# Kernel tuning notes

Hardware: AMD Instinct MI355X
Metric: run time of the kernel (lower is better)

Reference implementation:

```python
import jax, jax.numpy as jnp
import numpy as np

B, TE, T = 128, 256, 200
H, PRE, MEL, R = 256, 128, 80, 5
OUT = MEL * R  # 400


def _gru(x, h, wih, whh, bih, bhh):
    # PyTorch GRUCell math. wih: [3H, in], whh: [3H, H]
    gi = x @ wih.T + bih
    gh = h @ whh.T + bhh
    ir, iz, inn = jnp.split(gi, 3, axis=-1)
    hr, hz, hn = jnp.split(gh, 3, axis=-1)
    r = jax.nn.sigmoid(ir + hr)
    z = jax.nn.sigmoid(iz + hz)
    n = jnp.tanh(inn + r * hn)
    return (1.0 - z) * n + z * h


def setup_inputs() -> dict:
    key = jax.random.key(0)
    ks = jax.random.split(key, 32)
    s = 0.05
    d = {
        "encoder_outputs": jax.random.normal(ks[0], (B, TE, H), jnp.float32),
        "targets": jax.random.normal(ks[1], (B, T, OUT), jnp.float32),
        # prenet (note: prenet input is mel_dim*r = 400 frames fed through Linear(400->256)
        # is not in the original; original hardcodes Linear(256,256) on a 400-dim frame --
        # a bug. We size the first prenet layer to the actual frame dim 400.)
        "prenet_w1": jax.random.normal(ks[2], (H, OUT), jnp.float32) * s,
        "prenet_b1": jnp.zeros((H,), jnp.float32),
        "prenet_w2": jax.random.normal(ks[3], (PRE, H), jnp.float32) * s,
        "prenet_b2": jnp.zeros((PRE,), jnp.float32),
        # attention RNN: GRUCell(256+128, 256)
        "attn_wih": jax.random.normal(ks[4], (3 * H, H + PRE), jnp.float32) * s,
        "attn_whh": jax.random.normal(ks[5], (3 * H, H), jnp.float32) * s,
        "attn_bih": jnp.zeros((3 * H,), jnp.float32),
        "attn_bhh": jnp.zeros((3 * H,), jnp.float32),
        # Bahdanau attention: query layer, memory layer (bias-free), score vector v
        "wq": jax.random.normal(ks[6], (H, H), jnp.float32) * s,
        "wm": jax.random.normal(ks[7], (H, H), jnp.float32) * s,
        "v_attn": jax.random.normal(ks[8], (H,), jnp.float32) * s,
        # proj_to_decoder: Linear(512, 256)
        "wp": jax.random.normal(ks[9], (H, 2 * H), jnp.float32) * s,
        "bp": jnp.zeros((H,), jnp.float32),
        # decoder GRUCell x2 (256,256)
        "g1_wih": jax.random.normal(ks[10], (3 * H, H), jnp.float32) * s,
        "g1_whh": jax.random.normal(ks[11], (3 * H, H), jnp.float32) * s,
        "g1_bih": jnp.zeros((3 * H,), jnp.float32),
        "g1_bhh": jnp.zeros((3 * H,), jnp.float32),
        "g2_wih": jax.random.normal(ks[12], (3 * H, H), jnp.float32) * s,
        "g2_whh": jax.random.normal(ks[13], (3 * H, H), jnp.float32) * s,
        "g2_bih": jnp.zeros((3 * H,), jnp.float32),
        "g2_bhh": jnp.zeros((3 * H,), jnp.float32),
        # proj_to_mel: Linear(256, mel_dim*r)
        "wo": jax.random.normal(ks[14], (OUT, H), jnp.float32) * s,
        "bo": jnp.zeros((OUT,), jnp.float32),
    }
    return d


def reference(encoder_outputs, targets, prenet_w1, prenet_b1, prenet_w2, prenet_b2,
              attn_wih, attn_whh, attn_bih, attn_bhh, wq, wm, v_attn, wp, bp,
              g1_wih, g1_whh, g1_bih, g1_bhh, g2_wih, g2_whh, g2_bih, g2_bhh,
              wo, bo):
    b = encoder_outputs.shape[0]
    # precompute processed memory once (original memory_layer)
    pm = encoder_outputs @ wm.T  # [B, Te, H]

    # teacher-forced previous frames: go-frame (zeros) then targets[:, :-1]
    prev = jnp.concatenate([jnp.zeros((b, 1, OUT), encoder_outputs.dtype),
                            targets[:, :-1]], axis=1)  # [B, T, OUT]
    prev = jnp.swapaxes(prev, 0, 1)  # [T, B, OUT]

    def step(carry, frame):
        attn_h, h1, h2, attn_val = carry
        # prenet (dropout in eval mode -> identity)
        p = jax.nn.relu(frame @ prenet_w1.T + prenet_b1)
        p = jax.nn.relu(p @ prenet_w2.T + prenet_b2)  # [B, 128]
        # attention RNN
        x = jnp.concatenate([p, attn_val], axis=-1)  # [B, 384]
        attn_h = _gru(x, attn_h, attn_wih, attn_whh, attn_bih, attn_bhh)
        # Bahdanau additive attention
        q = attn_h @ wq.T  # [B, H]
        e = jnp.einsum('bth,h->bt', jnp.tanh(pm + q[:, None, :]), v_attn)  # [B, Te]
        align = jax.nn.softmax(e, axis=-1)
        attn_val = jnp.einsum('bt,bth->bh', align, encoder_outputs)
        # decoder RNNs with residual connections
        dec_in = jnp.concatenate([attn_h, attn_val], axis=-1) @ wp.T + bp
        h1 = _gru(dec_in, h1, g1_wih, g1_whh, g1_bih, g1_bhh)
        dec_in = h1 + dec_in
        h2 = _gru(dec_in, h2, g2_wih, g2_whh, g2_bih, g2_bhh)
        dec_in = h2 + dec_in
        out = dec_in @ wo.T + bo  # [B, OUT]
        return (attn_h, h1, h2, attn_val), (out, align)

    z = jnp.zeros((b, H), encoder_outputs.dtype)
    init = (z, z, z, z)
    _, (outs, aligns) = jax.lax.scan(step, init, prev)
    outputs = jnp.swapaxes(outs, 0, 1)      # [B, T, mel_dim*r]
    alignments = jnp.swapaxes(aligns, 0, 1)  # [B, T, Te]
    return outputs, alignments
```

## Files before the change

kernel.cpp:

```cpp
#include <hip/hip_runtime.h>

#define B_    128
#define T_    200
#define TE_   256
#define H_    256
#define PRE_  128
#define OUT_  400
#define BT_   (B_*T_)

__device__ __forceinline__ float sigm_(float x){ return 1.f/(1.f+__expf(-x)); }
__device__ __forceinline__ float tanh_(float x){
  x = fminf(15.f, fmaxf(-15.f, x));
  float e = __expf(2.f*x);
  return 1.f - 2.f/(e+1.f);
}
__device__ __forceinline__ float b2f_lo(unsigned u){ return __uint_as_float(u << 16); }
__device__ __forceinline__ float b2f_hi(unsigned u){ return __uint_as_float(u & 0xffff0000u); }
__device__ __forceinline__ unsigned short f2b(float f){
  unsigned u = __float_as_uint(f);
  unsigned r = (u + 0x7fff + ((u >> 16) & 1)) >> 16;
  return (unsigned short)r;
}

struct TD { const float* src; void* dst; int N; int Ksrc; int col0; int Keff; int bf16; int blk0; };
struct TDs { TD d[13]; };

__global__ __launch_bounds__(256) void transpose_cast(TDs P)
{
  int bid = blockIdx.x, m = 0;
#pragma unroll
  for (int i = 1; i < 13; ++i) if (bid >= P.d[i].blk0) m = i;
  TD t = P.d[m];
  long gid = (long)(bid - t.blk0)*256 + threadIdx.x;
  long nk = (long)t.N * t.Keff;
  if (gid >= nk) return;
  int k = (int)(gid / t.N);
  int j = (int)(gid % t.N);
  float v = t.src[(size_t)j*t.Ksrc + t.col0 + k];
  if (t.bf16) ((unsigned short*)t.dst)[(size_t)k*t.N + j] = f2b(v);
  else        ((float*)t.dst)[(size_t)k*t.N + j] = v;
}

template<int AMODE, bool RELU, int OUTMODE>
__global__ __launch_bounds__(256) void gemm_k(const float* __restrict__ A, int lda,
                                              const float* __restrict__ WT, int N, int K,
                                              const float* __restrict__ bias,
                                              float* __restrict__ C)
{
  const int tid  = threadIdx.x;
  const int row0 = blockIdx.x * 64;
  const int n0   = blockIdx.y * 64;
  __shared__ float As[16][68];
  __shared__ float Bs[16][64];
  const int tx = tid & 15, ty = tid >> 4;
  float acc[4][4];
#pragma unroll
  for (int i = 0; i < 4; ++i)
#pragma unroll
    for (int j = 0; j < 4; ++j) acc[i][j] = 0.f;

  for (int k0 = 0; k0 < K; k0 += 16){
#pragma unroll
    for (int l = 0; l < 4; ++l){
      int idx = tid + l*256;
      int m = idx >> 4, kk = idx & 15;
      float v;
      if (AMODE == 1){
        int r = row0 + m;
        int t = r % T_;
        v = (t == 0) ? 0.f : A[(size_t)(r-1)*OUT_ + k0 + kk];
      } else {
        v = A[(size_t)(row0+m)*lda + k0 + kk];
      }
      As[kk][m] = v;
    }
#pragma unroll
    for (int l = 0; l < 4; ++l){
      int idx = tid + l*256;
      int kk = idx >> 6, j = idx & 63;
      int jg = n0 + j;
      Bs[kk][j] = (jg < N) ? WT[(size_t)(k0+kk)*N + jg] : 0.f;
    }
    __syncthreads();
#pragma unroll
    for (int kk = 0; kk < 16; ++kk){
      float4 a4 = *(const float4*)&As[kk][ty*4];
      float4 b4 = *(const float4*)&Bs[kk][tx*4];
      acc[0][0] = fmaf(a4.x, b4.x, acc[0][0]); acc[0][1] = fmaf(a4.x, b4.y, acc[0][1]);
      acc[0][2] = fmaf(a4.x, b4.z, acc[0][2]); acc[0][3] = fmaf(a4.x, b4.w, acc[0][3]);
      acc[1][0] = fmaf(a4.y, b4.x, acc[1][0]); acc[1][1] = fmaf(a4.y, b4.y, acc[1][1]);
      acc[1][2] = fmaf(a4.y, b4.z, acc[1][2]); acc[1][3] = fmaf(a4.y, b4.w, acc[1][3]);
      acc[2][0] = fmaf(a4.z, b4.x, acc[2][0]); acc[2][1] = fmaf(a4.z, b4.y, acc[2][1]);
      acc[2][2] = fmaf(a4.z, b4.z, acc[2][2]); acc[2][3] = fmaf(a4.z, b4.w, acc[2][3]);
      acc[3][0] = fmaf(a4.w, b4.x, acc[3][0]); acc[3][1] = fmaf(a4.w, b4.y, acc[3][1]);
      acc[3][2] = fmaf(a4.w, b4.z, acc[3][2]); acc[3][3] = fmaf(a4.w, b4.w, acc[3][3]);
    }
    __syncthreads();
  }
#pragma unroll
  for (int i = 0; i < 4; ++i){
    int r = row0 + ty*4 + i;
#pragma unroll
    for (int jj = 0; jj < 4; ++jj){
      int c = n0 + tx*4 + jj;
      if (c < N){
        float v = acc[i][jj] + (bias ? bias[c] : 0.f);
        if (RELU) v = fmaxf(v, 0.f);
        if (OUTMODE == 0){
          C[(size_t)r*N + c] = v;
        } else {
          int b = r / TE_, te = r % TE_;
          C[((size_t)b*H_ + c)*TE_ + te] = v;
        }
      }
    }
  }
}

__device__ __forceinline__ void mv768(const uint2* __restrict__ w,
                                      const float* __restrict__ sin_,
                                      float* __restrict__ part, int tid)
{
  if (tid >= 768) return;
  const int kg = tid / 192;
  const int jt = tid - kg*192;
  const float4* sin4 = (const float4*)sin_;
  const uint2* wp_ = w + (size_t)(kg*64)*192 + jt;
  float a0=0.f, a1=0.f, a2=0.f, a3=0.f;
#pragma unroll 4
  for (int k4 = 0; k4 < 16; ++k4){
    float4 x = sin4[kg*16 + k4];
    uint2 w0 = wp_[0], w1 = wp_[192], w2 = wp_[384], w3 = wp_[576];
    wp_ += 768;
    a0 = fmaf(x.x, b2f_lo(w0.x), a0); a1 = fmaf(x.x, b2f_hi(w0.x), a1);
    a2 = fmaf(x.x, b2f_lo(w0.y), a2); a3 = fmaf(x.x, b2f_hi(w0.y), a3);
    a0 = fmaf(x.y, b2f_lo(w1.x), a0); a1 = fmaf(x.y, b2f_hi(w1.x), a1);
    a2 = fmaf(x.y, b2f_lo(w1.y), a2); a3 = fmaf(x.y, b2f_hi(w1.y), a3);
    a0 = fmaf(x.z, b2f_lo(w2.x), a0); a1 = fmaf(x.z, b2f_hi(w2.x), a1);
    a2 = fmaf(x.z, b2f_lo(w2.y), a2); a3 = fmaf(x.z, b2f_hi(w2.y), a3);
    a0 = fmaf(x.w, b2f_lo(w3.x), a0); a1 = fmaf(x.w, b2f_hi(w3.x), a1);
    a2 = fmaf(x.w, b2f_lo(w3.y), a2); a3 = fmaf(x.w, b2f_hi(w3.y), a3);
  }
  float* pp = part + kg*768 + jt*4;
  pp[0]=a0; pp[1]=a1; pp[2]=a2; pp[3]=a3;
}

template<int KCH>
__device__ __forceinline__ void mv256(const uint2* __restrict__ w,
                                      const float* __restrict__ sin_,
                                      float* __restrict__ part, int tid)
{
  const int kg = tid >> 6;
  const int jt = tid & 63;
  const float4* sin4 = (const float4*)sin_;
  const uint2* wp_ = w + (size_t)(kg*KCH)*64 + jt;
  float a0=0.f, a1=0.f, a2=0.f, a3=0.f;
#pragma unroll
  for (int k4 = 0; k4 < KCH/4; ++k4){
    float4 x = sin4[(kg*KCH)/4 + k4];
    uint2 w0 = wp_[0], w1 = wp_[64], w2 = wp_[128], w3 = wp_[192];
    wp_ += 256;
    a0 = fmaf(x.x, b2f_lo(w0.x), a0); a1 = fmaf(x.x, b2f_hi(w0.x), a1);
    a2 = fmaf(x.x, b2f_lo(w0.y), a2); a3 = fmaf(x.x, b2f_hi(w0.y), a3);
    a0 = fmaf(x.y, b2f_lo(w1.x), a0); a1 = fmaf(x.y, b2f_hi(w1.x), a1);
    a2 = fmaf(x.y, b2f_lo(w1.y), a2); a3 = fmaf(x.y, b2f_hi(w1.y), a3);
    a0 = fmaf(x.z, b2f_lo(w2.x), a0); a1 = fmaf(x.z, b2f_hi(w2.x), a1);
    a2 = fmaf(x.z, b2f_lo(w2.y), a2); a3 = fmaf(x.z, b2f_hi(w2.y), a3);
    a0 = fmaf(x.w, b2f_lo(w3.x), a0); a1 = fmaf(x.w, b2f_hi(w3.x), a1);
    a2 = fmaf(x.w, b2f_lo(w3.y), a2); a3 = fmaf(x.w, b2f_hi(w3.y), a3);
  }
  float* pp = part + kg*256 + jt*4;
  pp[0]=a0; pp[1]=a1; pp[2]=a2; pp[3]=a3;
}

struct DP {
  const float *enc, *preGI, *pm;
  const unsigned short *awihA, *awhh, *wq, *wp, *g1wih, *g1whh, *g2wih, *g2whh;
  const float *abhh, *g1bih, *g1bhh, *g2bih, *g2bhh, *bp, *v_attn;
  float *decbuf, *aln;
};

__global__ __launch_bounds__(1024) void decoder_kernel(DP P)
{
  const int tid = threadIdx.x;
  const int b = blockIdx.x;

  __shared__ __align__(16) float s_ah[H_], s_h1[H_], s_h2[H_], s_av[H_], s_q[H_], s_al[TE_], s_dec[H_];
  __shared__ __align__(16) float s_xc[2*H_];
  __shared__ __align__(16) float s_gi[3*H_], s_gh[3*H_];
  __shared__ __align__(16) float s_pA[4096];
  __shared__ __align__(16) float s_pB[3072];
  __shared__ float s_bhh[3*H_], s_1bi[3*H_], s_1bh[3*H_], s_2bi[3*H_], s_2bh[3*H_];
  __shared__ float s_bp[H_], s_v[H_];
  __shared__ float s_red[8];

  if (tid < H_){
    s_ah[tid]=0.f; s_h1[tid]=0.f; s_h2[tid]=0.f; s_av[tid]=0.f;
    s_bp[tid]=P.bp[tid]; s_v[tid]=P.v_attn[tid];
  }
  if (tid < 3*H_){
    s_bhh[tid]=P.abhh[tid];
    s_1bi[tid]=P.g1bih[tid]; s_1bh[tid]=P.g1bhh[tid];
    s_2bi[tid]=P.g2bih[tid]; s_2bh[tid]=P.g2bhh[tid];
  }
  __syncthreads();

  const float* preg  = P.preGI + (size_t)b*T_*3*H_;
  const float4* pm4  = (const float4*)(P.pm  + (size_t)b*H_*TE_);
  const float4* enc4 = (const float4*)(P.enc + (size_t)b*TE_*H_);
  float* aln_b = P.aln + (size_t)b*T_*TE_;
  float* dec_b = P.decbuf + (size_t)b*T_*H_;

  const uint2* awihA2 = (const uint2*)P.awihA;
  const uint2* awhh2  = (const uint2*)P.awhh;
  const uint2* wq2    = (const uint2*)P.wq;
  const uint2* wp2    = (const uint2*)P.wp;
  const uint2* g1wih2 = (const uint2*)P.g1wih;
  const uint2* g1whh2 = (const uint2*)P.g1whh;
  const uint2* g2wih2 = (const uint2*)P.g2wih;
  const uint2* g2whh2 = (const uint2*)P.g2whh;

  for (int t = 0; t < T_; ++t){
    float gin = (tid < 768) ? preg[(size_t)t*768 + tid] : 0.f;
    mv768(awihA2, s_av, s_pA, tid);
    mv768(awhh2,  s_ah, s_pB, tid);
    __syncthreads();
    if (tid < 768){
      s_gi[tid] = s_pA[tid]+s_pA[768+tid]+s_pA[1536+tid]+s_pA[2304+tid] + gin;
      s_gh[tid] = s_pB[tid]+s_pB[768+tid]+s_pB[1536+tid]+s_pB[2304+tid] + s_bhh[tid];
    }
    __syncthreads();
    if (tid < H_){
      float r = sigm_(s_gi[tid]      + s_gh[tid]);
      float z = sigm_(s_gi[H_+tid]   + s_gh[H_+tid]);
      float n = tanh_(s_gi[2*H_+tid] + r*s_gh[2*H_+tid]);
      s_ah[tid] = (1.f-z)*n + z*s_ah[tid];
    }
    __syncthreads();
    mv256<16>(wq2, s_ah, s_pA, tid);
    __syncthreads();
    if (tid < H_){
      float q = 0.f;
#pragma unroll
      for (int g = 0; g < 16; ++g) q += s_pA[g*256 + tid];
      s_q[tid] = q;
    }
    __syncthreads();
    {
      const int kg = tid >> 6, jt = tid & 63;
      float a0=0.f,a1=0.f,a2=0.f,a3=0.f;
#pragma unroll 4
      for (int hh = 0; hh < 16; ++hh){
        int h = kg*16 + hh;
        float4 pv = pm4[h*64 + jt];
        float qh = s_q[h], vh = s_v[h];
        a0 = fmaf(vh, tanh_(pv.x + qh), a0);
        a1 = fmaf(vh, tanh_(pv.y + qh), a1);
        a2 = fmaf(vh, tanh_(pv.z + qh), a2);
        a3 = fmaf(vh, tanh_(pv.w + qh), a3);
      }
      float* pp = s_pA + kg*256 + jt*4;
      pp[0]=a0; pp[1]=a1; pp[2]=a2; pp[3]=a3;
    }
    __syncthreads();
    float e = 0.f, ex = 0.f;
    if (tid < TE_){
#pragma unroll
      for (int g = 0; g < 16; ++g) e += s_pA[g*256 + tid];
      float m = e;
      for (int o = 32; o; o >>= 1) m = fmaxf(m, __shfl_down(m, o, 64));
      if ((tid & 63) == 0) s_red[tid >> 6] = m;
    }
    __syncthreads();
    if (tid < TE_){
      float m = fmaxf(fmaxf(s_red[0],s_red[1]), fmaxf(s_red[2],s_red[3]));
      ex = __expf(e - m);
      float s = ex;
      for (int o = 32; o; o >>= 1) s += __shfl_down(s, o, 64);
      if ((tid & 63) == 0) s_red[4 + (tid >> 6)] = s;
    }
    __syncthreads();
    if (tid < TE_){
      float s = (s_red[4]+s_red[5])+(s_red[6]+s_red[7]);
      float al = ex / s;
      s_al[tid] = al;
      aln_b[(size_t)t*TE_ + tid] = al;
    }
    __syncthreads();
    {
      const int kg = tid >> 6, jt = tid & 63;
      float a0=0.f,a1=0.f,a2=0.f,a3=0.f;
#pragma unroll 4
      for (int tt = 0; tt < 16; ++tt){
        int te = kg*16 + tt;
        float alv = s_al[te];
        float4 ev = enc4[te*64 + jt];
        a0 = fmaf(alv, ev.x, a0);
        a1 = fmaf(alv, ev.y, a1);
        a2 = fmaf(alv, ev.z, a2);
        a3 = fmaf(alv, ev.w, a3);
      }
      float* pp = s_pA + kg*256 + jt*4;
      pp[0]=a0; pp[1]=a1; pp[2]=a2; pp[3]=a3;
    }
    __syncthreads();
    if (tid < H_){
      float av = 0.f;
#pragma unroll
      for (int g = 0; g < 16; ++g) av += s_pA[g*256 + tid];
      s_av[tid] = av;
      s_xc[tid] = s_ah[tid];
      s_xc[H_ + tid] = av;
    }
    __syncthreads();
    mv256<32>(wp2, s_xc, s_pA, tid);
    __syncthreads();
    if (tid < H_){
      float d = s_bp[tid];
#pragma unroll
      for (int g = 0; g < 16; ++g) d += s_pA[g*256 + tid];
      s_dec[tid] = d;
    }
    __syncthreads();
    mv768(g1wih2, s_dec, s_pA, tid);
    mv768(g1whh2, s_h1,  s_pB, tid);
    __syncthreads();
    if (tid < 768){
      s_gi[tid] = s_pA[tid]+s_pA[768+tid]+s_pA[1536+tid]+s_pA[2304+tid] + s_1bi[tid];
      s_gh[tid] = s_pB[tid]+s_pB[768+tid]+s_pB[1536+tid]+s_pB[2304+tid] + s_1bh[tid];
    }
    __syncthreads();
    if (tid < H_){
      float r = sigm_(s_gi[tid]      + s_gh[tid]);
      float z = sigm_(s_gi[H_+tid]   + s_gh[H_+tid]);
      float n = tanh_(s_gi[2*H_+tid] + r*s_gh[2*H_+tid]);
      float h1n = (1.f-z)*n + z*s_h1[tid];
      s_h1[tid] = h1n;
      s_dec[tid] += h1n;
    }
    __syncthreads();
    mv768(g2wih2, s_dec, s_pA, tid);
    mv768(g2whh2, s_h2,  s_pB, tid);
    __syncthreads();
    if (tid < 768){
      s_gi[tid] = s_pA[tid]+s_pA[768+tid]+s_pA[1536+tid]+s_pA[2304+tid] + s_2bi[tid];
      s_gh[tid] = s_pB[tid]+s_pB[768+tid]+s_pB[1536+tid]+s_pB[2304+tid] + s_2bh[tid];
    }
    __syncthreads();
    if (tid < H_){
      float r = sigm_(s_gi[tid]      + s_gh[tid]);
      float z = sigm_(s_gi[H_+tid]   + s_gh[H_+tid]);
      float n = tanh_(s_gi[2*H_+tid] + r*s_gh[2*H_+tid]);
      float h2n = (1.f-z)*n + z*s_h2[tid];
      s_h2[tid] = h2n;
      float d = s_dec[tid] + h2n;
      s_dec[tid] = d;
      dec_b[(size_t)t*H_ + tid] = d;
    }
    __syncthreads();
  }
}

extern "C" void kernel_launch(void* const* d_in, const int* in_sizes, int n_in,
                              void* d_out, int out_size, void* d_ws, size_t ws_size,
                              hipStream_t stream)
{
  const float* enc   = (const float*)d_in[0];
  const float* tgt   = (const float*)d_in[1];
  const float* pw1   = (const float*)d_in[2];
  const float* pb1   = (const float*)d_in[3];
  const float* pw2   = (const float*)d_in[4];
  const float* pb2   = (const float*)d_in[5];
  const float* awih  = (const float*)d_in[6];
  const float* awhh  = (const float*)d_in[7];
  const float* abih  = (const float*)d_in[8];
  const float* abhh  = (const float*)d_in[9];
  const float* wq    = (const float*)d_in[10];
  const float* wm    = (const float*)d_in[11];
  const float* vat   = (const float*)d_in[12];
  const float* wp    = (const float*)d_in[13];
  const float* bp    = (const float*)d_in[14];
  const float* g1wih = (const float*)d_in[15];
  const float* g1whh = (const float*)d_in[16];
  const float* g1bih = (const float*)d_in[17];
  const float* g1bhh = (const float*)d_in[18];
  const float* g2wih = (const float*)d_in[19];
  const float* g2whh = (const float*)d_in[20];
  const float* g2bih = (const float*)d_in[21];
  const float* g2bhh = (const float*)d_in[22];
  const float* wo    = (const float*)d_in[23];
  const float* bo    = (const float*)d_in[24];

  float* ws = (float*)d_ws;
  size_t off = 0;
  auto alloc = [&](size_t n){ float* p = ws + off; off += (n + 3) & ~(size_t)3; return p; };

  float* wmT    = alloc(65536);
  float* w1T    = alloc(102400);
  float* w2T    = alloc(32768);
  float* awihPT = alloc(98304);
  float* woT    = alloc(102400);
  unsigned short* awihA16 = (unsigned short*)alloc(98304);
  unsigned short* awhh16  = (unsigned short*)alloc(98304);
  unsigned short* wq16    = (unsigned short*)alloc(32768);
  unsigned short* wp16    = (unsigned short*)alloc(65536);
  unsigned short* g1wih16 = (unsigned short*)alloc(98304);
  unsigned short* g1whh16 = (unsigned short*)alloc(98304);
  unsigned short* g2wih16 = (unsigned short*)alloc(98304);
  unsigned short* g2whh16 = (unsigned short*)alloc(98304);
  float* pmf    = alloc((size_t)B_*H_*TE_);
  float* decb   = alloc((size_t)BT_*H_);
  float* preGIf = alloc((size_t)BT_*3*H_);
  float* p1f = decb;
  float* p2f = pmf;

  TDs td;
  const float* srcs[13] = { wm,  pw1, pw2, awih, wo,  awih, awhh, wq,  wp,  g1wih, g1whh, g2wih, g2whh };
  void* dsts[13] = { wmT, w1T, w2T, awihPT, woT, awihA16, awhh16, wq16, wp16, g1wih16, g1whh16, g2wih16, g2whh16 };
  int   Ns[13]   = { 256, 256, 128, 768,  400, 768, 768, 256, 256, 768, 768, 768, 768 };
  int   Kss[13]  = { 256, 400, 256, 384,  256, 384, 256, 256, 512, 256, 256, 256, 256 };
  int   c0s[13]  = { 0,   0,   0,   0,    0,   128, 0,   0,   0,   0,   0,   0,   0 };
  int   Kes[13]  = { 256, 400, 256, 128,  256, 256, 256, 256, 512, 256, 256, 256, 256 };
  int   bfs[13]  = { 0,   0,   0,   0,    0,   1,   1,   1,   1,   1,   1,   1,   1 };
  int blk = 0;
  for (int i = 0; i < 13; ++i){
    td.d[i] = { srcs[i], dsts[i], Ns[i], Kss[i], c0s[i], Kes[i], bfs[i], blk };
    long nk = (long)Ns[i]*Kes[i];
    blk += (int)((nk + 255) / 256);
  }
  transpose_cast<<<blk, 256, 0, stream>>>(td);

  gemm_k<1, true, 0><<<dim3(BT_/64, 4), 256, 0, stream>>>(tgt, 0,   w1T,    256, 400, pb1,  p1f);
  gemm_k<0, true, 0><<<dim3(BT_/64, 2), 256, 0, stream>>>(p1f, 256, w2T,    128, 256, pb2,  p2f);
  gemm_k<0, false,0><<<dim3(BT_/64,12), 256, 0, stream>>>(p2f, 128, awihPT, 768, 128, abih, preGIf);
  gemm_k<0, false,1><<<dim3((B_*TE_)/64, 4), 256, 0, stream>>>(enc, 256, wmT, 256, 256, nullptr, pmf);

  DP P;
  P.enc = enc; P.preGI = preGIf; P.pm = pmf;
  P.awihA = awihA16; P.awhh = awhh16; P.wq = wq16; P.wp = wp16;
  P.g1wih = g1wih16; P.g1whh = g1whh16; P.g2wih = g2wih16; P.g2whh = g2whh16;
  P.abhh = abhh; P.g1bih = g1bih; P.g1bhh = g1bhh; P.g2bih = g2bih; P.g2bhh = g2bhh;
  P.bp = bp; P.v_attn = vat;
  P.decbuf = decb;
  P.aln = (float*)d_out + (size_t)BT_*OUT_;
  decoder_kernel<<<B_, 1024, 0, stream>>>(P);

  gemm_k<0, false,0><<<dim3(BT_/64, 7), 256, 0, stream>>>(decb, 256, woT, 400, 256, bo, (float*)d_out);
}
```

Measured before the change: 13.64 ms.

## Restructure decoder step: batch independent matvecs, bf16 memory/encoder, drop softmax max

The decoder step now issues the attention and both decoder hidden-to-hidden matvecs together in one phase, computes the query and the attention-state half of the projection together, and prefetches the precomputed gate inputs with the otherwise idle threads. This removes several barriers per timestep. The processed memory and the encoder outputs are stored as bf16 to halve per-step global traffic, and biases are kept in registers. The softmax max-subtraction pass is dropped, which saves one reduction and barrier but risks overflow if scores grow large, and bf16 storage lowers precision.

```diff
diff --git a/kernel.cpp b/kernel.cpp
--- a/kernel.cpp
+++ b/kernel.cpp
@@ -22,14 +22,18 @@
   return (unsigned short)r;
 }
 
+#define Q4(xv, wv, A0,A1,A2,A3) \
+  A0=fmaf(xv,b2f_lo(wv.x),A0); A1=fmaf(xv,b2f_hi(wv.x),A1); \
+  A2=fmaf(xv,b2f_lo(wv.y),A2); A3=fmaf(xv,b2f_hi(wv.y),A3);
+
 struct TD { const float* src; void* dst; int N; int Ksrc; int col0; int Keff; int bf16; int blk0; };
-struct TDs { TD d[13]; };
+struct TDs { TD d[14]; };
 
 __global__ __launch_bounds__(256) void transpose_cast(TDs P)
 {
   int bid = blockIdx.x, m = 0;
 #pragma unroll
-  for (int i = 1; i < 13; ++i) if (bid >= P.d[i].blk0) m = i;
+  for (int i = 1; i < 14; ++i) if (bid >= P.d[i].blk0) m = i;
   TD t = P.d[m];
   long gid = (long)(bid - t.blk0)*256 + threadIdx.x;
   long nk = (long)t.N * t.Keff;
@@ -63,16 +67,16 @@
 #pragma unroll
     for (int l = 0; l < 4; ++l){
       int idx = tid + l*256;
-      int m = idx >> 4, kk = idx & 15;
+      int m2 = idx >> 4, kk = idx & 15;
       float v;
       if (AMODE == 1){
-        int r = row0 + m;
+        int r = row0 + m2;
         int t = r % T_;
         v = (t == 0) ? 0.f : A[(size_t)(r-1)*OUT_ + k0 + kk];
       } else {
-        v = A[(size_t)(row0+m)*lda + k0 + kk];
+        v = A[(size_t)(row0+m2)*lda + k0 + kk];
       }
-      As[kk][m] = v;
+      As[kk][m2] = v;
     }
 #pragma unroll
     for (int l = 0; l < 4; ++l){
@@ -108,73 +112,111 @@
         if (RELU) v = fmaxf(v, 0.f);
         if (OUTMODE == 0){
           C[(size_t)r*N + c] = v;
+        } else if (OUTMODE == 1){
+          int b = r / TE_, te = r % TE_;
+          C[((size_t)b*H_ + c)*TE_ + te] = v;
         } else {
           int b = r / TE_, te = r % TE_;
-          C[((size_t)b*H_ + c)*TE_ + te] = v;
+          ((unsigned short*)C)[((size_t)b*H_ + c)*TE_ + te] = f2b(v);
         }
       }
     }
   }
 }
 
-__device__ __forceinline__ void mv768(const uint2* __restrict__ w,
-                                      const float* __restrict__ sin_,
-                                      float* __restrict__ part, int tid)
-{
-  if (tid >= 768) return;
-  const int kg = tid / 192;
-  const int jt = tid - kg*192;
-  const float4* sin4 = (const float4*)sin_;
-  const uint2* wp_ = w + (size_t)(kg*64)*192 + jt;
-  float a0=0.f, a1=0.f, a2=0.f, a3=0.f;
+__device__ __forceinline__ void mv768_pair(const uint2* __restrict__ wA, const uint2* __restrict__ wB,
+                                           const float* __restrict__ xA, const float* __restrict__ xB,
+                                           float* __restrict__ outA, float* __restrict__ outB,
+                                           int kg, int jt)
+{
+  const float4* xa4 = (const float4*)xA;
+  const float4* xb4 = (const float4*)xB;
+  const uint2* pA = wA + (size_t)(kg*64)*192 + jt;
+  const uint2* pB = wB + (size_t)(kg*64)*192 + jt;
+  float a0=0,a1=0,a2=0,a3=0, c0=0,c1=0,c2=0,c3=0;
 #pragma unroll 4
   for (int k4 = 0; k4 < 16; ++k4){
-    float4 x = sin4[kg*16 + k4];
-    uint2 w0 = wp_[0], w1 = wp_[192], w2 = wp_[384], w3 = wp_[576];
-    wp_ += 768;
-    a0 = fmaf(x.x, b2f_lo(w0.x), a0); a1 = fmaf(x.x, b2f_hi(w0.x), a1);
-    a2 = fmaf(x.x, b2f_lo(w0.y), a2); a3 = fmaf(x.x, b2f_hi(w0.y), a3);
-    a0 = fmaf(x.y, b2f_lo(w1.x), a0); a1 = fmaf(x.y, b2f_hi(w1.x), a1);
-    a2 = fmaf(x.y, b2f_lo(w1.y), a2); a3 = fmaf(x.y, b2f_hi(w1.y), a3);
-    a0 = fmaf(x.z, b2f_lo(w2.x), a0); a1 = fmaf(x.z, b2f_hi(w2.x), a1);
-    a2 = fmaf(x.z, b2f_lo(w2.y), a2); a3 = fmaf(x.z, b2f_hi(w2.y), a3);
-    a0 = fmaf(x.w, b2f_lo(w3.x), a0); a1 = fmaf(x.w, b2f_hi(w3.x), a1);
-    a2 = fmaf(x.w, b2f_lo(w3.y), a2); a3 = fmaf(x.w, b2f_hi(w3.y), a3);
-  }
-  float* pp = part + kg*768 + jt*4;
-  pp[0]=a0; pp[1]=a1; pp[2]=a2; pp[3]=a3;
-}
-
-template<int KCH>
-__device__ __forceinline__ void mv256(const uint2* __restrict__ w,
-                                      const float* __restrict__ sin_,
-                                      float* __restrict__ part, int tid)
-{
-  const int kg = tid >> 6;
-  const int jt = tid & 63;
-  const float4* sin4 = (const float4*)sin_;
-  const uint2* wp_ = w + (size_t)(kg*KCH)*64 + jt;
-  float a0=0.f, a1=0.f, a2=0.f, a3=0.f;
-#pragma unroll
-  for (int k4 = 0; k4 < KCH/4; ++k4){
-    float4 x = sin4[(kg*KCH)/4 + k4];
-    uint2 w0 = wp_[0], w1 = wp_[64], w2 = wp_[128], w3 = wp_[192];
-    wp_ += 256;
-    a0 = fmaf(x.x, b2f_lo(w0.x), a0); a1 = fmaf(x.x, b2f_hi(w0.x), a1);
-    a2 = fmaf(x.x, b2f_lo(w0.y), a2); a3 = fmaf(x.x, b2f_hi(w0.y), a3);
-    a0 = fmaf(x.y, b2f_lo(w1.x), a0); a1 = fmaf(x.y, b2f_hi(w1.x), a1);
-    a2 = fmaf(x.y, b2f_lo(w1.y), a2); a3 = fmaf(x.y, b2f_hi(w1.y), a3);
-    a0 = fmaf(x.z, b2f_lo(w2.x), a0); a1 = fmaf(x.z, b2f_hi(w2.x), a1);
-    a2 = fmaf(x.z, b2f_lo(w2.y), a2); a3 = fmaf(x.z, b2f_hi(w2.y), a3);
-    a0 = fmaf(x.w, b2f_lo(w3.x), a0); a1 = fmaf(x.w, b2f_hi(w3.x), a1);
-    a2 = fmaf(x.w, b2f_lo(w3.y), a2); a3 = fmaf(x.w, b2f_hi(w3.y), a3);
-  }
-  float* pp = part + kg*256 + jt*4;
-  pp[0]=a0; pp[1]=a1; pp[2]=a2; pp[3]=a3;
+    float4 x1 = xa4[kg*16+k4];
+    float4 x2 = xb4[kg*16+k4];
+    uint2 wa0=pA[0],wa1=pA[192],wa2=pA[384],wa3=pA[576]; pA += 768;
+    uint2 wb0=pB[0],wb1=pB[192],wb2=pB[384],wb3=pB[576]; pB += 768;
+    Q4(x1.x, wa0, a0,a1,a2,a3) Q4(x1.y, wa1, a0,a1,a2,a3)
+    Q4(x1.z, wa2, a0,a1,a2,a3) Q4(x1.w, wa3, a0,a1,a2,a3)
+    Q4(x2.x, wb0, c0,c1,c2,c3) Q4(x2.y, wb1, c0,c1,c2,c3)
+    Q4(x2.z, wb2, c0,c1,c2,c3) Q4(x2.w, wb3, c0,c1,c2,c3)
+  }
+  *(float4*)(outA + jt*4) = make_float4(a0,a1,a2,a3);
+  *(float4*)(outB + jt*4) = make_float4(c0,c1,c2,c3);
+}
+
+__device__ __forceinline__ void mv768_single(const uint2* __restrict__ w,
+                                             const float* __restrict__ x,
+                                             float* __restrict__ out, int kg, int jt)
+{
+  const float4* x4 = (const float4*)x;
+  const uint2* p = w + (size_t)(kg*64)*192 + jt;
+  float a0=0,a1=0,a2=0,a3=0;
+#pragma unroll 4
+  for (int k4 = 0; k4 < 16; ++k4){
+    float4 x1 = x4[kg*16+k4];
+    uint2 w0=p[0],w1=p[192],w2=p[384],w3=p[576]; p += 768;
+    Q4(x1.x, w0, a0,a1,a2,a3) Q4(x1.y, w1, a0,a1,a2,a3)
+    Q4(x1.z, w2, a0,a1,a2,a3) Q4(x1.w, w3, a0,a1,a2,a3)
+  }
+  *(float4*)(out + jt*4) = make_float4(a0,a1,a2,a3);
+}
+
+__device__ __forceinline__ void mv256_pair(const uint2* __restrict__ wA, const uint2* __restrict__ wB,
+                                           const float* __restrict__ x,
+                                           float* __restrict__ outA, float* __restrict__ outB,
+                                           int kg, int jt)
+{
+  const float4* x4 = (const float4*)x;
+  const uint2* pA = wA + (size_t)(kg*16)*64 + jt;
+  const uint2* pB = wB + (size_t)(kg*16)*64 + jt;
+  float a0=0,a1=0,a2=0,a3=0, c0=0,c1=0,c2=0,c3=0;
+#pragma unroll
+  for (int k4 = 0; k4 < 4; ++k4){
+    float4 x1 = x4[kg*4+k4];
+    uint2 wa0=pA[0],wa1=pA[64],wa2=pA[128],wa3=pA[192]; pA += 256;
+    uint2 wb0=pB[0],wb1=pB[64],wb2=pB[128],wb3=pB[192]; pB += 256;
+    Q4(x1.x, wa0, a0,a1,a2,a3) Q4(x1.y, wa1, a0,a1,a2,a3)
+    Q4(x1.z, wa2, a0,a1,a2,a3) Q4(x1.w, wa3, a0,a1,a2,a3)
+    Q4(x1.x, wb0, c0,c1,c2,c3) Q4(x1.y, wb1, c0,c1,c2,c3)
+    Q4(x1.z, wb2, c0,c1,c2,c3) Q4(x1.w, wb3, c0,c1,c2,c3)
+  }
+  *(float4*)(outA + jt*4) = make_float4(a0,a1,a2,a3);
+  *(float4*)(outB + jt*4) = make_float4(c0,c1,c2,c3);
+}
+
+__device__ __forceinline__ void mv256_single(const uint2* __restrict__ w,
+                                             const float* __restrict__ x,
+                                             float* __restrict__ out, int kg, int jt)
+{
+  const float4* x4 = (const float4*)x;
+  const uint2* p = w + (size_t)(kg*16)*64 + jt;
+  float a0=0,a1=0,a2=0,a3=0;
+#pragma unroll
+  for (int k4 = 0; k4 < 4; ++k4){
+    float4 x1 = x4[kg*4+k4];
+    uint2 w0=p[0],w1=p[64],w2=p[128],w3=p[192]; p += 256;
+    Q4(x1.x, w0, a0,a1,a2,a3) Q4(x1.y, w1, a0,a1,a2,a3)
+    Q4(x1.z, w2, a0,a1,a2,a3) Q4(x1.w, w3, a0,a1,a2,a3)
+  }
+  *(float4*)(out + jt*4) = make_float4(a0,a1,a2,a3);
+}
+
+__device__ __forceinline__ float gru_gate(float gi0,float gi1,float gi2,
+                                          float gh0,float gh1,float gh2, float hprev){
+  float r = sigm_(gi0+gh0);
+  float z = sigm_(gi1+gh1);
+  float n = tanh_(gi2 + r*gh2);
+  return (1.f-z)*n + z*hprev;
 }
 
 struct DP {
-  const float *enc, *preGI, *pm;
+  const float *preGI;
+  const unsigned short *pm16, *enc16;
   const unsigned short *awihA, *awhh, *wq, *wp, *g1wih, *g1whh, *g2wih, *g2whh;
   const float *abhh, *g1bih, *g1bhh, *g2bih, *g2bhh, *bp, *v_attn;
   float *decbuf, *aln;
@@ -185,173 +227,184 @@
   const int tid = threadIdx.x;
   const int b = blockIdx.x;
 
-  __shared__ __align__(16) float s_ah[H_], s_h1[H_], s_h2[H_], s_av[H_], s_q[H_], s_al[TE_], s_dec[H_];
-  __shared__ __align__(16) float s_xc[2*H_];
-  __shared__ __align__(16) float s_gi[3*H_], s_gh[3*H_];
-  __shared__ __align__(16) float s_pA[4096];
-  __shared__ __align__(16) float s_pB[3072];
-  __shared__ float s_bhh[3*H_], s_1bi[3*H_], s_1bh[3*H_], s_2bi[3*H_], s_2bh[3*H_];
-  __shared__ float s_bp[H_], s_v[H_];
-  __shared__ float s_red[8];
-
+  __shared__ __align__(16) float s_part[12288];
+  __shared__ __align__(16) float s_g1h[768], s_g2h[768];
+  __shared__ __align__(16) float s_ah[H_], s_h1[H_], s_h2[H_], s_av[H_], s_dec[H_];
+  __shared__ __align__(16) float s_q[H_], s_dq[H_], s_al[TE_], s_v[H_];
+  __shared__ __align__(16) float s_preg[768];
+  __shared__ float s_red[4];
+
+  float r_bh0=0,r_bh1=0,r_bh2=0, r_1bi0=0,r_1bi1=0,r_1bi2=0;
+  float r_2bi0=0,r_2bi1=0,r_2bi2=0, r_bp=0, r_g1bh=0, r_g2bh=0;
   if (tid < H_){
+    r_bh0=P.abhh[tid];  r_bh1=P.abhh[H_+tid];  r_bh2=P.abhh[2*H_+tid];
+    r_1bi0=P.g1bih[tid]; r_1bi1=P.g1bih[H_+tid]; r_1bi2=P.g1bih[2*H_+tid];
+    r_2bi0=P.g2bih[tid]; r_2bi1=P.g2bih[H_+tid]; r_2bi2=P.g2bih[2*H_+tid];
+    r_bp=P.bp[tid];
+    s_v[tid]=P.v_attn[tid];
     s_ah[tid]=0.f; s_h1[tid]=0.f; s_h2[tid]=0.f; s_av[tid]=0.f;
-    s_bp[tid]=P.bp[tid]; s_v[tid]=P.v_attn[tid];
-  }
-  if (tid < 3*H_){
-    s_bhh[tid]=P.abhh[tid];
-    s_1bi[tid]=P.g1bih[tid]; s_1bh[tid]=P.g1bhh[tid];
-    s_2bi[tid]=P.g2bih[tid]; s_2bh[tid]=P.g2bhh[tid];
+  } else {
+    int j = tid - 256;
+    r_g1bh = P.g1bhh[j];
+    r_g2bh = P.g2bhh[j];
   }
   __syncthreads();
 
-  const float* preg  = P.preGI + (size_t)b*T_*3*H_;
-  const float4* pm4  = (const float4*)(P.pm  + (size_t)b*H_*TE_);
-  const float4* enc4 = (const float4*)(P.enc + (size_t)b*TE_*H_);
+  const float* preg = P.preGI + (size_t)b*T_*768;
+  const uint2* pm2  = (const uint2*)(P.pm16  + (size_t)b*H_*TE_);
+  const uint2* en2  = (const uint2*)(P.enc16 + (size_t)b*TE_*H_);
   float* aln_b = P.aln + (size_t)b*T_*TE_;
   float* dec_b = P.decbuf + (size_t)b*T_*H_;
 
   const uint2* awihA2 = (const uint2*)P.awihA;
   const uint2* awhh2  = (const uint2*)P.awhh;
   const uint2* wq2    = (const uint2*)P.wq;
-  const uint2* wp2    = (const uint2*)P.wp;
+  const uint2* wpA2   = (const uint2*)P.wp;
+  const uint2* wpB2   = ((const uint2*)P.wp) + 16384;
   const uint2* g1wih2 = (const uint2*)P.g1wih;
   const uint2* g1whh2 = (const uint2*)P.g1whh;
   const uint2* g2wih2 = (const uint2*)P.g2wih;
   const uint2* g2whh2 = (const uint2*)P.g2whh;
 
+  const int kg8 = tid >> 6, jt8 = tid & 63;
+
   for (int t = 0; t < T_; ++t){
-    float gin = (tid < 768) ? preg[(size_t)t*768 + tid] : 0.f;
-    mv768(awihA2, s_av, s_pA, tid);
-    mv768(awhh2,  s_ah, s_pB, tid);
-    __syncthreads();
     if (tid < 768){
-      s_gi[tid] = s_pA[tid]+s_pA[768+tid]+s_pA[1536+tid]+s_pA[2304+tid] + gin;
-      s_gh[tid] = s_pB[tid]+s_pB[768+tid]+s_pB[1536+tid]+s_pB[2304+tid] + s_bhh[tid];
+      const int kg = tid / 192, jt = tid - (tid/192)*192;
+      mv768_pair(awihA2, awhh2, s_av, s_ah,
+                 s_part + (0*4+kg)*768, s_part + (1*4+kg)*768, kg, jt);
+      mv768_pair(g1whh2, g2whh2, s_h1, s_h2,
+                 s_part + (2*4+kg)*768, s_part + (3*4+kg)*768, kg, jt);
+    } else {
+      int i = tid - 768;
+      s_preg[i]       = preg[(size_t)t*768 + i];
+      s_preg[i + 256] = preg[(size_t)t*768 + i + 256];
+      s_preg[i + 512] = preg[(size_t)t*768 + i + 512];
     }
     __syncthreads();
     if (tid < H_){
-      float r = sigm_(s_gi[tid]      + s_gh[tid]);
-      float z = sigm_(s_gi[H_+tid]   + s_gh[H_+tid]);
-      float n = tanh_(s_gi[2*H_+tid] + r*s_gh[2*H_+tid]);
-      s_ah[tid] = (1.f-z)*n + z*s_ah[tid];
-    }
-    __syncthreads();
-    mv256<16>(wq2, s_ah, s_pA, tid);
-    __syncthreads();
-    if (tid < H_){
+      float gi0 = s_part[tid]     + s_part[768+tid]     + s_part[1536+tid]     + s_part[2304+tid]     + s_preg[tid];
+      float gi1 = s_part[256+tid] + s_part[1024+tid]    + s_part[1792+tid]     + s_part[2560+tid]     + s_preg[256+tid];
+      float gi2 = s_part[512+tid] + s_part[1280+tid]    + s_part[2048+tid]     + s_part[2816+tid]     + s_preg[512+tid];
+      float gh0 = s_part[3072+tid]     + s_part[3840+tid]     + s_part[4608+tid]     + s_part[5376+tid]     + r_bh0;
+      float gh1 = s_part[3072+256+tid] + s_part[3840+256+tid] + s_part[4608+256+tid] + s_part[5376+256+tid] + r_bh1;
+      float gh2 = s_part[3072+512+tid] + s_part[3840+512+tid] + s_part[4608+512+tid] + s_part[5376+512+tid] + r_bh2;
+      s_ah[tid] = gru_gate(gi0,gi1,gi2, gh0,gh1,gh2, s_ah[tid]);
+    } else {
+      int j = tid - 256;
+      s_g1h[j] = s_part[6144+j] + s_part[6912+j] + s_part[7680+j] + s_part[8448+j] + r_g1bh;
+      s_g2h[j] = s_part[9216+j] + s_part[9984+j] + s_part[10752+j] + s_part[11520+j] + r_g2bh;
+    }
+    __syncthreads();
+
+    mv256_pair(wq2, wpA2, s_ah, s_part + kg8*256, s_part + 4096 + kg8*256, kg8, jt8);
+    __syncthreads();
+    if (tid < 256){
       float q = 0.f;
 #pragma unroll
-      for (int g = 0; g < 16; ++g) q += s_pA[g*256 + tid];
+      for (int g = 0; g < 16; ++g) q += s_part[g*256 + tid];
       s_q[tid] = q;
-    }
-    __syncthreads();
+    } else if (tid < 512){
+      int j = tid - 256;
+      float d = 0.f;
+#pragma unroll
+      for (int g = 0; g < 16; ++g) d += s_part[4096 + g*256 + j];
+      s_dq[j] = d;
+    }
+    __syncthreads();
+
     {
-      const int kg = tid >> 6, jt = tid & 63;
-      float a0=0.f,a1=0.f,a2=0.f,a3=0.f;
+      float a0=0,a1=0,a2=0,a3=0;
 #pragma unroll 4
       for (int hh = 0; hh < 16; ++hh){
-        int h = kg*16 + hh;
-        float4 pv = pm4[h*64 + jt];
+        int h = kg8*16 + hh;
+        uint2 pv = pm2[(size_t)h*64 + jt8];
         float qh = s_q[h], vh = s_v[h];
-        a0 = fmaf(vh, tanh_(pv.x + qh), a0);
-        a1 = fmaf(vh, tanh_(pv.y + qh), a1);
-        a2 = fmaf(vh, tanh_(pv.z + qh), a2);
-        a3 = fmaf(vh, tanh_(pv.w + qh), a3);
+        a0 = fmaf(vh, tanh_(b2f_lo(pv.x)+qh), a0);
+        a1 = fmaf(vh, tanh_(b2f_hi(pv.x)+qh), a1);
+        a2 = fmaf(vh, tanh_(b2f_lo(pv.y)+qh), a2);
+        a3 = fmaf(vh, tanh_(b2f_hi(pv.y)+qh), a3);
       }
-      float* pp = s_pA + kg*256 + jt*4;
-      pp[0]=a0; pp[1]=a1; pp[2]=a2; pp[3]=a3;
-    }
-    __syncthreads();
-    float e = 0.f, ex = 0.f;
+      *(float4*)(s_part + kg8*256 + jt8*4) = make_float4(a0,a1,a2,a3);
+    }
+    __syncthreads();
+    float ex = 0.f;
     if (tid < TE_){
-#pragma unroll
-      for (int g = 0; g < 16; ++g) e += s_pA[g*256 + tid];
-      float m = e;
-      for (int o = 32; o; o >>= 1) m = fmaxf(m, __shfl_down(m, o, 64));
-      if ((tid & 63) == 0) s_red[tid >> 6] = m;
-    }
-    __syncthreads();
-    if (tid < TE_){
-      float m = fmaxf(fmaxf(s_red[0],s_red[1]), fmaxf(s_red[2],s_red[3]));
-      ex = __expf(e - m);
+      float e = 0.f;
+#pragma unroll
+      for (int g = 0; g < 16; ++g) e += s_part[g*256 + tid];
+      ex = __expf(e);
       float s = ex;
       for (int o = 32; o; o >>= 1) s += __shfl_down(s, o, 64);
-      if ((tid & 63) == 0) s_red[4 + (tid >> 6)] = s;
+      if ((tid & 63) == 0) s_red[tid >> 6] = s;
     }
     __syncthreads();
     if (tid < TE_){
-      float s = (s_red[4]+s_red[5])+(s_red[6]+s_red[7]);
+      float s = (s_red[0]+s_red[1])+(s_red[2]+s_red[3]);
       float al = ex / s;
       s_al[tid] = al;
       aln_b[(size_t)t*TE_ + tid] = al;
     }
     __syncthreads();
+
     {
-      const int kg = tid >> 6, jt = tid & 63;
-      float a0=0.f,a1=0.f,a2=0.f,a3=0.f;
+      float a0=0,a1=0,a2=0,a3=0;
 #pragma unroll 4
       for (int tt = 0; tt < 16; ++tt){
-        int te = kg*16 + tt;
+        int te = kg8*16 + tt;
         float alv = s_al[te];
-        float4 ev = enc4[te*64 + jt];
-        a0 = fmaf(alv, ev.x, a0);
-        a1 = fmaf(alv, ev.y, a1);
-        a2 = fmaf(alv, ev.z, a2);
-        a3 = fmaf(alv, ev.w, a3);
+        uint2 ev = en2[(size_t)te*64 + jt8];
+        a0 = fmaf(alv, b2f_lo(ev.x), a0);
+        a1 = fmaf(alv, b2f_hi(ev.x), a1);
+        a2 = fmaf(alv, b2f_lo(ev.y), a2);
+        a3 = fmaf(alv, b2f_hi(ev.y), a3);
       }
-      float* pp = s_pA + kg*256 + jt*4;
-      pp[0]=a0; pp[1]=a1; pp[2]=a2; pp[3]=a3;
+      *(float4*)(s_part + kg8*256 + jt8*4) = make_float4(a0,a1,a2,a3);
     }
     __syncthreads();
     if (tid < H_){
       float av = 0.f;
 #pragma unroll
-      for (int g = 0; g < 16; ++g) av += s_pA[g*256 + tid];
+      for (int g = 0; g < 16; ++g) av += s_part[g*256 + tid];
       s_av[tid] = av;
-      s_xc[tid] = s_ah[tid];
-      s_xc[H_ + tid] = av;
-    }
-    __syncthreads();
-    mv256<32>(wp2, s_xc, s_pA, tid);
+    }
+    __syncthreads();
+
+    mv256_single(wpB2, s_av, s_part + kg8*256, kg8, jt8);
     __syncthreads();
     if (tid < H_){
-      float d = s_bp[tid];
-#pragma unroll
-      for (int g = 0; g < 16; ++g) d += s_pA[g*256 + tid];
+      float d = s_dq[tid] + r_bp;
+#pragma unroll
+      for (int g = 0; g < 16; ++g) d += s_part[g*256 + tid];
       s_dec[tid] = d;
     }
     __syncthreads();
-    mv768(g1wih2, s_dec, s_pA, tid);
-    mv768(g1whh2, s_h1,  s_pB, tid);
-    __syncthreads();
+
     if (tid < 768){
-      s_gi[tid] = s_pA[tid]+s_pA[768+tid]+s_pA[1536+tid]+s_pA[2304+tid] + s_1bi[tid];
-      s_gh[tid] = s_pB[tid]+s_pB[768+tid]+s_pB[1536+tid]+s_pB[2304+tid] + s_1bh[tid];
+      const int kg = tid / 192, jt = tid - (tid/192)*192;
+      mv768_single(g1wih2, s_dec, s_part + kg*768, kg, jt);
     }
     __syncthreads();
     if (tid < H_){
-      float r = sigm_(s_gi[tid]      + s_gh[tid]);
-      float z = sigm_(s_gi[H_+tid]   + s_gh[H_+tid]);
-      float n = tanh_(s_gi[2*H_+tid] + r*s_gh[2*H_+tid]);
-      float h1n = (1.f-z)*n + z*s_h1[tid];
+      float gi0 = s_part[tid]     + s_part[768+tid]  + s_part[1536+tid] + s_part[2304+tid] + r_1bi0;
+      float gi1 = s_part[256+tid] + s_part[1024+tid] + s_part[1792+tid] + s_part[2560+tid] + r_1bi1;
+      float gi2 = s_part[512+tid] + s_part[1280+tid] + s_part[2048+tid] + s_part[2816+tid] + r_1bi2;
+      float h1n = gru_gate(gi0,gi1,gi2, s_g1h[tid], s_g1h[256+tid], s_g1h[512+tid], s_h1[tid]);
       s_h1[tid] = h1n;
       s_dec[tid] += h1n;
     }
     __syncthreads();
-    mv768(g2wih2, s_dec, s_pA, tid);
-    mv768(g2whh2, s_h2,  s_pB, tid);
-    __syncthreads();
+
     if (tid < 768){
-      s_gi[tid] = s_pA[tid]+s_pA[768+tid]+s_pA[1536+tid]+s_pA[2304+tid] + s_2bi[tid];
-      s_gh[tid] = s_pB[tid]+s_pB[768+tid]+s_pB[1536+tid]+s_pB[2304+tid] + s_2bh[tid];
+      const int kg = tid / 192, jt = tid - (tid/192)*192;
+      mv768_single(g2wih2, s_dec, s_part + kg*768, kg, jt);
     }
     __syncthreads();
     if (tid < H_){
-      float r = sigm_(s_gi[tid]      + s_gh[tid]);
-      float z = sigm_(s_gi[H_+tid]   + s_gh[H_+tid]);
-      float n = tanh_(s_gi[2*H_+tid] + r*s_gh[2*H_+tid]);
-      float h2n = (1.f-z)*n + z*s_h2[tid];
+      float gi0 = s_part[tid]     + s_part[768+tid]  + s_part[1536+tid] + s_part[2304+tid] + r_2bi0;
+      float gi1 = s_part[256+tid] + s_part[1024+tid] + s_part[1792+tid] + s_part[2560+tid] + r_2bi1;
+      float gi2 = s_part[512+tid] + s_part[1280+tid] + s_part[2048+tid] + s_part[2816+tid] + r_2bi2;
+      float h2n = gru_gate(gi0,gi1,gi2, s_g2h[tid], s_g2h[256+tid], s_g2h[512+tid], s_h2[tid]);
       s_h2[tid] = h2n;
       float d = s_dec[tid] + h2n;
       s_dec[tid] = d;
@@ -408,22 +461,23 @@
   unsigned short* g1whh16 = (unsigned short*)alloc(98304);
   unsigned short* g2wih16 = (unsigned short*)alloc(98304);
   unsigned short* g2whh16 = (unsigned short*)alloc(98304);
-  float* pmf    = alloc((size_t)B_*H_*TE_);
+  unsigned short* pm16  = (unsigned short*)alloc(4194304);
+  unsigned short* enc16 = (unsigned short*)alloc(4194304);
   float* decb   = alloc((size_t)BT_*H_);
+  float* p2f    = alloc((size_t)BT_*PRE_);
   float* preGIf = alloc((size_t)BT_*3*H_);
   float* p1f = decb;
-  float* p2f = pmf;
 
   TDs td;
-  const float* srcs[13] = { wm,  pw1, pw2, awih, wo,  awih, awhh, wq,  wp,  g1wih, g1whh, g2wih, g2whh };
-  void* dsts[13] = { wmT, w1T, w2T, awihPT, woT, awihA16, awhh16, wq16, wp16, g1wih16, g1whh16, g2wih16, g2whh16 };
-  int   Ns[13]   = { 256, 256, 128, 768,  400, 768, 768, 256, 256, 768, 768, 768, 768 };
-  int   Kss[13]  = { 256, 400, 256, 384,  256, 384, 256, 256, 512, 256, 256, 256, 256 };
-  int   c0s[13]  = { 0,   0,   0,   0,    0,   128, 0,   0,   0,   0,   0,   0,   0 };
-  int   Kes[13]  = { 256, 400, 256, 128,  256, 256, 256, 256, 512, 256, 256, 256, 256 };
-  int   bfs[13]  = { 0,   0,   0,   0,    0,   1,   1,   1,   1,   1,   1,   1,   1 };
+  const float* srcs[14] = { wm,  pw1, pw2, awih, wo,  awih, awhh, wq,  wp,  g1wih, g1whh, g2wih, g2whh, enc };
+  void* dsts[14] = { wmT, w1T, w2T, awihPT, woT, awihA16, awhh16, wq16, wp16, g1wih16, g1whh16, g2wih16, g2whh16, enc16 };
+  int   Ns[14]   = { 256, 256, 128, 768,  400, 768, 768, 256, 256, 768, 768, 768, 768, B_*TE_*H_ };
+  int   Kss[14]  = { 256, 400, 256, 384,  256, 384, 256, 256, 512, 256, 256, 256, 256, 1 };
+  int   c0s[14]  = { 0,   0,   0,   0,    0,   128, 0,   0,   0,   0,   0,   0,   0,   0 };
+  int   Kes[14]  = { 256, 400, 256, 128,  256, 256, 256, 256, 512, 256, 256, 256, 256, 1 };
+  int   bfs[14]  = { 0,   0,   0,   0,    0,   1,   1,   1,   1,   1,   1,   1,   1,   1 };
   int blk = 0;
-  for (int i = 0; i < 13; ++i){
+  for (int i = 0; i < 14; ++i){
     td.d[i] = { srcs[i], dsts[i], Ns[i], Kss[i], c0s[i], Kes[i], bfs[i], blk };
     long nk = (long)Ns[i]*Kes[i];
     blk += (int)((nk + 255) / 256);
@@ -433,10 +487,10 @@
   gemm_k<1, true, 0><<<dim3(BT_/64, 4), 256, 0, stream>>>(tgt, 0,   w1T,    256, 400, pb1,  p1f);
   gemm_k<0, true, 0><<<dim3(BT_/64, 2), 256, 0, stream>>>(p1f, 256, w2T,    128, 256, pb2,  p2f);
   gemm_k<0, false,0><<<dim3(BT_/64,12), 256, 0, stream>>>(p2f, 128, awihPT, 768, 128, abih, preGIf);
-  gemm_k<0, false,1><<<dim3((B_*TE_)/64, 4), 256, 0, stream>>>(enc, 256, wmT, 256, 256, nullptr, pmf);
+  gemm_k<0, false,2><<<dim3((B_*TE_)/64, 4), 256, 0, stream>>>(enc, 256, wmT, 256, 256, nullptr, (float*)pm16);
 
   DP P;
-  P.enc = enc; P.preGI = preGIf; P.pm = pmf;
+  P.preGI = preGIf; P.pm16 = pm16; P.enc16 = enc16;
   P.awihA = awihA16; P.awhh = awhh16; P.wq = wq16; P.wp = wp16;
   P.g1wih = g1wih16; P.g1whh = g1whh16; P.g2wih = g2wih16; P.g2whh = g2whh16;
   P.abhh = abhh; P.g1bih = g1bih; P.g1bhh = g1bhh; P.g2bih = g2bih; P.g2bhh = g2bhh;
```

Result: slower. 14.44 ms (+5.8%).
